# Kernel optimization log

Measured on AMD Instinct MI355X. Metric: run time of the kernel, lower is better.

Reference implementation:

```python
import jax, jax.numpy as jnp
import numpy as np

BATCH, D, Q = 8192, 256, 16

def setup_inputs() -> dict:
    key = jax.random.key(0)
    X = jax.random.normal(key, (BATCH, D, Q), dtype=jnp.float32)
    return {"X": X}

def reference(X):
    # Re-orthonormalization: thin QR, return the orthonormal factor Q (batch, d, q)
    Qm, _R = jnp.linalg.qr(X, mode="reduced")
    return Qm
```

## Files before the change

### kernel.cpp

```cpp
#include <hip/hip_runtime.h>


constexpr int BATCH = 8192;
constexpr int DROWS = 256;
constexpr int QC    = 16;

__device__ __forceinline__ float rdlane(float v, int l) {
    return __int_as_float(__builtin_amdgcn_readlane(__float_as_int(v), l));
}

template <int CTRL>
__device__ __forceinline__ float dpp_add(float x) {
    int y = __builtin_amdgcn_update_dpp(0, __float_as_int(x), CTRL, 0xf, 0xf, true);
    return x + __int_as_float(y);
}

__device__ __forceinline__ float wave_sum64(float x) {
    x = dpp_add<0xB1>(x);
    x = dpp_add<0x4E>(x);
    x = dpp_add<0x141>(x);
    x = dpp_add<0x140>(x);
    x = dpp_add<0x142>(x);
    x = dpp_add<0x143>(x);
    return rdlane(x, 63);
}

__device__ __forceinline__ float wave_sum32(float x) {
    x = dpp_add<0xB1>(x);
    x = dpp_add<0x4E>(x);
    x = dpp_add<0x141>(x);
    x = dpp_add<0x140>(x);
    x = dpp_add<0x142>(x);
    return rdlane(x, 31);
}

__global__ __launch_bounds__(256, 4) void qr_cholhh_kernel(
    const float* __restrict__ in, float* __restrict__ out)
{
    const int lane = threadIdx.x & 63;
    const int wid  = threadIdx.x >> 6;
    const int b    = blockIdx.x * 4 + wid;

    const float4* __restrict__ A4 = (const float4*)(in  + (size_t)b * (DROWS * QC));
    float4*       __restrict__ O4 = (float4*)      (out + (size_t)b * (DROWS * QC));

    float x[4][QC];

#pragma unroll
    for (int s = 0; s < 4; ++s) {
        const int rr = s * 64 + lane;
#pragma unroll
        for (int q4 = 0; q4 < 4; ++q4) {
            float4 t = A4[rr * 4 + q4];
            x[s][q4*4+0] = t.x; x[s][q4*4+1] = t.y;
            x[s][q4*4+2] = t.z; x[s][q4*4+3] = t.w;
        }
    }

    const int li = lane - 16;

    float xm[QC];
#pragma unroll
    for (int i = 0; i < QC; ++i) xm[i] = (lane < 16) ? 0.f : x[0][i];

    float g[QC];
#pragma unroll
    for (int i = 0; i < QC; ++i) g[i] = 0.f;

#pragma unroll
    for (int j = 0; j < QC; ++j) {
#pragma unroll
        for (int i = 0; i <= j; ++i) {
            float p = fmaf(x[3][i], x[3][j],
                      fmaf(x[2][i], x[2][j],
                      fmaf(x[1][i], x[1][j], xm[i] * x[0][j])));
            const float sv = wave_sum64(p);
            g[j] = (li == i) ? sv : g[j];
            if (i != j) g[i] = (li == j) ? sv : g[i];
        }
    }

    float rs = 0.f;
#pragma unroll
    for (int k = 0; k < QC; ++k) {
        const float piv = rdlane(g[k], 16 + k);
        const float inv = __builtin_amdgcn_rcpf(piv);
        const float rsk = __builtin_amdgcn_rsqf(piv);
        rs = (li == k) ? rsk : rs;
        const float m = (li > k) ? g[k] * inv : 0.f;
#pragma unroll
        for (int j = k + 1; j < QC; ++j) {
            const float bj = rdlane(g[j], 16 + k);
            g[j] = fmaf(-m, bj, g[j]);
        }
    }

    float c[QC];
#pragma unroll
    for (int t = 0; t < QC; ++t) {
        const float ub = (li <= t) ? g[t] * rs : 0.f;
        c[t] = (lane < 16) ? x[0][t] : ub;
    }

    float nrm2[QC];
#pragma unroll
    for (int t = 0; t < QC; ++t) nrm2[t] = wave_sum32(c[t] * c[t]);

#pragma unroll
    for (int j = 0; j < QC; ++j) {
        const float piv   = rdlane(c[j], j);
        const float nrm   = sqrtf(nrm2[j]);
        const float alpha = -copysignf(nrm, piv);
        const float vtv   = 2.f * (nrm2[j] - alpha * piv);
        const float beta  = 2.f * __builtin_amdgcn_rcpf(vtv);
        const float v = (lane < j) ? 0.f : ((lane == j) ? piv - alpha : c[j]);
#pragma unroll
        for (int t = j + 1; t < QC; ++t) {
            const float d  = wave_sum32(v * c[t]);
            const float wb = beta * d;
            c[t] = fmaf(-wb, v, c[t]);
            const float rv = rdlane(c[t], j);
            nrm2[t] = fmaf(-rv, rv, nrm2[t]);
        }
        c[j] = (lane == j) ? alpha : c[j];
    }

#pragma unroll
    for (int k = 0; k < QC; ++k) {
        const float rkk = rdlane(c[k], k);
        const float ikk = __builtin_amdgcn_rcpf(rkk);
        x[0][k] *= ikk; x[1][k] *= ikk; x[2][k] *= ikk; x[3][k] *= ikk;
#pragma unroll
        for (int t = k + 1; t < QC; ++t) {
            const float r = rdlane(c[t], k);
            x[0][t] = fmaf(-r, x[0][k], x[0][t]);
            x[1][t] = fmaf(-r, x[1][k], x[1][t]);
            x[2][t] = fmaf(-r, x[2][k], x[2][t]);
            x[3][t] = fmaf(-r, x[3][k], x[3][t]);
        }
    }

#pragma unroll
    for (int s = 0; s < 4; ++s) {
        const int rr = s * 64 + lane;
#pragma unroll
        for (int q4 = 0; q4 < 4; ++q4) {
            O4[rr * 4 + q4] = make_float4(x[s][q4*4+0], x[s][q4*4+1],
                                          x[s][q4*4+2], x[s][q4*4+3]);
        }
    }
}

extern "C" void kernel_launch(void* const* d_in, const int* in_sizes, int n_in,
                              void* d_out, int out_size, void* d_ws, size_t ws_size,
                              hipStream_t stream) {
    const float* X = (const float*)d_in[0];
    float*       O = (float*)d_out;
    qr_cholhh_kernel<<<BATCH / 4, 256, 0, stream>>>(X, O);
}
```

Baseline: 264.5 us.

## Compute Gram matrix with split-fp16 MFMA instead of per-entry wave reductions

```diff
diff --git a/kernel.cpp b/kernel.cpp
--- a/kernel.cpp
+++ b/kernel.cpp
@@ -4,6 +4,9 @@
 constexpr int BATCH = 8192;
 constexpr int DROWS = 256;
 constexpr int QC    = 16;
+
+typedef _Float16 half8 __attribute__((ext_vector_type(8)));
+typedef float    f32x4 __attribute__((ext_vector_type(4)));
 
 __device__ __forceinline__ float rdlane(float v, int l) {
     return __int_as_float(__builtin_amdgcn_readlane(__float_as_int(v), l));
@@ -15,16 +18,6 @@
     return x + __int_as_float(y);
 }
 
-__device__ __forceinline__ float wave_sum64(float x) {
-    x = dpp_add<0xB1>(x);
-    x = dpp_add<0x4E>(x);
-    x = dpp_add<0x141>(x);
-    x = dpp_add<0x140>(x);
-    x = dpp_add<0x142>(x);
-    x = dpp_add<0x143>(x);
-    return rdlane(x, 63);
-}
-
 __device__ __forceinline__ float wave_sum32(float x) {
     x = dpp_add<0xB1>(x);
     x = dpp_add<0x4E>(x);
@@ -34,12 +27,16 @@
     return rdlane(x, 31);
 }
 
-__global__ __launch_bounds__(256, 4) void qr_cholhh_kernel(
+__global__ __launch_bounds__(256) void qr_mfma_r7(
     const float* __restrict__ in, float* __restrict__ out)
 {
     const int lane = threadIdx.x & 63;
     const int wid  = threadIdx.x >> 6;
     const int b    = blockIdx.x * 4 + wid;
+
+    __shared__ __align__(16) char smem[4][2 * QC * 72 * 2];
+    unsigned short* hp = reinterpret_cast<unsigned short*>(smem[wid]);
+    unsigned short* lp = hp + QC * 72;
 
     const float4* __restrict__ A4 = (const float4*)(in  + (size_t)b * (DROWS * QC));
     float4*       __restrict__ O4 = (float4*)      (out + (size_t)b * (DROWS * QC));
@@ -57,28 +54,53 @@
         }
     }
 
-    const int li = lane - 16;
+    f32x4 accA = {0.f, 0.f, 0.f, 0.f};
+    f32x4 accB = {0.f, 0.f, 0.f, 0.f};
+    const int cm   = lane & 15;
+    const int g4   = lane >> 4;
+    const int fidx = cm * 72 + 8 * g4;
 
-    float xm[QC];
 #pragma unroll
-    for (int i = 0; i < QC; ++i) xm[i] = (lane < 16) ? 0.f : x[0][i];
+    for (int s = 0; s < 4; ++s) {
+#pragma unroll
+        for (int c = 0; c < QC; ++c) {
+            float v = x[s][c];
+            if (s == 0) v = (lane < QC) ? 0.f : v;
+            _Float16 hh = (_Float16)v;
+            float     r = v - (float)hh;
+            _Float16 ll = (_Float16)r;
+            union { _Float16 f; unsigned short u; } ch, cl;
+            ch.f = hh; cl.f = ll;
+            hp[c * 72 + lane] = ch.u;
+            lp[c * 72 + lane] = cl.u;
+        }
+        asm volatile("" ::: "memory");
+#pragma unroll
+        for (int h = 0; h < 2; ++h) {
+            const half8 fh = *reinterpret_cast<const half8*>(&hp[fidx + 32 * h]);
+            const half8 fl = *reinterpret_cast<const half8*>(&lp[fidx + 32 * h]);
+            accA = __builtin_amdgcn_mfma_f32_16x16x32_f16(fh, fh, accA, 0, 0, 0);
+            accB = __builtin_amdgcn_mfma_f32_16x16x32_f16(fh, fl, accB, 0, 0, 0);
+            accB = __builtin_amdgcn_mfma_f32_16x16x32_f16(fl, fh, accB, 0, 0, 0);
+            accA = __builtin_amdgcn_mfma_f32_16x16x32_f16(fl, fl, accA, 0, 0, 0);
+        }
+        asm volatile("" ::: "memory");
+    }
+    const f32x4 Gf = accA + accB;
 
+    float* gbuf = reinterpret_cast<float*>(smem[wid]);
+    asm volatile("" ::: "memory");
+#pragma unroll
+    for (int q = 0; q < 4; ++q) gbuf[(4 * g4 + q) * 20 + cm] = Gf[q];
+    asm volatile("" ::: "memory");
     float g[QC];
 #pragma unroll
-    for (int i = 0; i < QC; ++i) g[i] = 0.f;
+    for (int k = 0; k < 4; ++k) {
+        const f32x4 t = *reinterpret_cast<const f32x4*>(&gbuf[(lane & 15) * 20 + 4 * k]);
+        g[4*k+0] = t[0]; g[4*k+1] = t[1]; g[4*k+2] = t[2]; g[4*k+3] = t[3];
+    }
 
-#pragma unroll
-    for (int j = 0; j < QC; ++j) {
-#pragma unroll
-        for (int i = 0; i <= j; ++i) {
-            float p = fmaf(x[3][i], x[3][j],
-                      fmaf(x[2][i], x[2][j],
-                      fmaf(x[1][i], x[1][j], xm[i] * x[0][j])));
-            const float sv = wave_sum64(p);
-            g[j] = (li == i) ? sv : g[j];
-            if (i != j) g[i] = (li == j) ? sv : g[i];
-        }
-    }
+    const int li = lane - 16;
 
     float rs = 0.f;
 #pragma unroll
@@ -98,8 +120,8 @@
     float c[QC];
 #pragma unroll
     for (int t = 0; t < QC; ++t) {
-        const float ub = (li <= t) ? g[t] * rs : 0.f;
-        c[t] = (lane < 16) ? x[0][t] : ub;
+        const float ub = (li <= t && li >= 0) ? g[t] * rs : 0.f;
+        c[t] = (lane < QC) ? x[0][t] : ub;
     }
 
     float nrm2[QC];
@@ -156,5 +178,5 @@
                               hipStream_t stream) {
     const float* X = (const float*)d_in[0];
     float*       O = (float*)d_out;
-    qr_cholhh_kernel<<<BATCH / 4, 256, 0, stream>>>(X, O);
+    qr_mfma_r7<<<BATCH / 4, 256, 0, stream>>>(X, O);
 }
```

Result: faster. 245.6 us (-7.2%).
